# Performance work log

Measured on AMD Instinct MI355X. Metric: run time of the kernel, lower is better.

The kernel has to match this reference:

```python
import jax, jax.numpy as jnp
from jax import lax
import numpy as np

B = 16
H0 = 56
W0 = 56
C = 768
HEADS = 12
SCALES = 3
WS = 7
LC = C // SCALES          # 256 local channels per scale group
HD = C // HEADS           # 64 head dim (= conv groups)
LH = HEADS // SCALES      # 4 local heads per group


def setup_inputs() -> dict:
    key = jax.random.key(0)
    ks = jax.random.split(key, 6)
    x = jax.random.normal(ks[0], (B, H0 * W0, C), jnp.float32)
    w_qkv = jax.random.normal(ks[1], (3 * C, C), jnp.float32) * 0.02
    w_proj = jax.random.normal(ks[2], (C, C), jnp.float32) * 0.02
    b_proj = jnp.zeros((C,), jnp.float32)
    # grouped conv (groups = head_dim = 64): weight (out=LC, in_per_group=LC//HD, 3, 3)
    conv1_w = jax.random.normal(ks[3], (LC, LC // HD, 3, 3), jnp.float32) * 0.05
    conv1_b = jnp.zeros((LC,), jnp.float32)
    conv2_w = jax.random.normal(ks[4], (LC, LC // HD, 3, 3), jnp.float32) * 0.05
    conv2_b = jnp.zeros((LC,), jnp.float32)
    return {"x": x, "w_qkv": w_qkv, "w_proj": w_proj, "b_proj": b_proj,
            "conv1_w": conv1_w, "conv1_b": conv1_b,
            "conv2_w": conv2_w, "conv2_b": conv2_b,
            "H": H0, "W": W0}


def _grouped_conv(xc, w, b, stride, pad, dil):
    y = lax.conv_general_dilated(
        xc, w, window_strides=(stride, stride),
        padding=((pad, pad), (pad, pad)), rhs_dilation=(dil, dil),
        feature_group_count=HD,
        dimension_numbers=("NCHW", "OIHW", "NCHW"))
    return y + b[None, :, None, None]


def _maxpool2(xc):
    return lax.reduce_window(xc, -jnp.inf, lax.max,
                             (1, 1, 2, 2), (1, 1, 2, 2), "VALID")


def _patchify(arr):
    # arr: (B, LC, Hs, Ws) -> (B*n_region, LH, WS*WS, HD)
    b, lc, hs, ws = arr.shape
    a = arr.reshape(b, lc, hs // WS, WS, ws // WS, WS)
    a = a.transpose(0, 2, 4, 3, 5, 1).reshape(-1, WS * WS, lc)
    a = a.reshape(-1, WS * WS, LH, lc // LH).transpose(0, 2, 1, 3)
    return a


def reference(x, w_qkv, w_proj, b_proj, conv1_w, conv1_b, conv2_w, conv2_b, H, W):
    scale = HD ** -0.5
    Bx, N, Cx = x.shape
    # (B, N, 3C) -> (B, H, W, 3, C) -> (B, 3, C, H, W)
    qkv = (x @ w_qkv.T).reshape(Bx, H, W, 3, Cx).transpose(0, 3, 4, 1, 2)
    N_g = (H // WS) * (W // WS)
    conv_params = [(conv1_w, conv1_b, 1, 1, 1), (conv2_w, conv2_b, 2, 2, 2)]
    outs = []
    for i in range(SCALES):
        g = qkv[:, :, i * LC:(i + 1) * LC]  # (B, 3, LC, H, W)
        Hs, Ws = H >> i, W >> i
        if i > 0:
            w, b, st, pd, dl = conv_params[i - 1]
            g = g.reshape(Bx * 3, LC, H, W)
            g = _maxpool2(_grouped_conv(g, w, b, st, pd, dl))
            g = g.reshape(Bx, 3, LC, Hs, Ws)
        q = _patchify(g[:, 0])
        k = _patchify(g[:, 1])
        v = _patchify(g[:, 2])
        attn = jax.nn.softmax(jnp.einsum("whpd,whqd->whpq", q, k) * scale, axis=-1)
        y = jnp.einsum("whpq,whqd->whpd", attn, v)  # (B*nreg, LH, 49, HD)
        nreg = (Hs // WS) * (Ws // WS)
        y = y.reshape(Bx, nreg, LH, WS * WS, HD).transpose(0, 2, 1, 3, 4)
        if i > 0:
            y = jnp.tile(y, (1, 1, N_g // nreg, 1, 1))
        outs.append(y)
    fused = jnp.concatenate(outs, axis=1)  # (B, HEADS, N_g, 49, HD)
    fused = fused.reshape(Bx, HEADS, -1, HD).transpose(0, 2, 1, 3).reshape(Bx, N, Cx)
    return fused @ w_proj.T + b_proj
```

## Files before the change

### kernel.cpp

```cpp
#include <hip/hip_runtime.h>

typedef __attribute__((ext_vector_type(4))) float f32x4;
typedef __attribute__((ext_vector_type(8))) short bf16x8;
typedef __attribute__((ext_vector_type(4))) unsigned short u16x4;
typedef unsigned short u16;

__device__ static u16   g_xh[(size_t)50176 * 768];
__device__ static u16   g_wqkvh[(size_t)2304 * 768];
__device__ static u16   g_wprojh[(size_t)768 * 768];
__device__ static u16   g_qkv[(size_t)50176 * 2304];
__device__ static u16   g_g1[(size_t)48 * 784 * 256];
__device__ static u16   g_g2[(size_t)48 * 196 * 256];
__device__ static u16   g_fh[(size_t)50176 * 768];

static __device__ __forceinline__ u16 f2bf(float x){
  unsigned u = __float_as_uint(x);
  u += 0x7fffu + ((u >> 16) & 1u);
  return (u16)(u >> 16);
}
static __device__ __forceinline__ float bf2f(u16 h){
  return __uint_as_float(((unsigned)h) << 16);
}

__global__ __launch_bounds__(256)
void cvt_bf16(const float* __restrict__ in, u16* __restrict__ out, int n4)
{
  int i = blockIdx.x * blockDim.x + threadIdx.x;
  const int stride = gridDim.x * blockDim.x;
  for (; i < n4; i += stride) {
    const f32x4 v = ((const f32x4*)in)[i];
    u16x4 o;
    #pragma unroll
    for (int j = 0; j < 4; j++) o[j] = f2bf(v[j]);
    ((u16x4*)out)[i] = o;
  }
}

template<bool BIAS, typename OUT_T>
__global__ __launch_bounds__(512, 2)
void gemm256(const u16* __restrict__ A0, const u16* __restrict__ Bw,
             const float* __restrict__ bias, OUT_T* __restrict__ C,
             int N, int K, int GX)
{
  __shared__ __align__(16) char ldsb[4 * 32768];
  const int tid = threadIdx.x;
  const int lane = tid & 63;
  const int w = tid >> 6;
  const int wm = w >> 2;
  const int wn = w & 3;
  const int l15 = lane & 15, l4 = lane >> 4;

  const int nwg = gridDim.x;
  const int bid = blockIdx.x;
  const int q8 = nwg >> 3, r8 = nwg & 7;
  const int xcd = bid & 7, lid = bid >> 3;
  const int swz = (xcd < r8 ? xcd * (q8 + 1) : r8 * (q8 + 1) + (xcd - r8) * q8) + lid;
  const int bn = swz % GX;
  const int bm = swz / GX;

  const int sq = tid >> 3;
  const int sp = tid & 7;
  const int tt = sp ^ (sq & 7);
  const int sa = tt >> 2, scc = tt & 3;
  const int srow0 = sq * 2 + sa;
  const u16* a0 = A0 + (size_t)(bm * 256 + srow0) * K + scc * 8;
  const u16* a1 = A0 + (size_t)(bm * 256 + 128 + srow0) * K + scc * 8;
  const u16* b0 = Bw + (size_t)(bn * 256 + srow0) * K + scc * 8;
  const u16* b1 = Bw + (size_t)(bn * 256 + 128 + srow0) * K + scc * 8;
  const int wofs = w << 10;

  #define GLDS(srcp, ldsoff) __builtin_amdgcn_global_load_lds( \
      (__attribute__((address_space(1))) const void*)(srcp),   \
      (__attribute__((address_space(3))) void*)(ldsb + (ldsoff)), 16, 0, 0)

  auto STAGE = [&](int s) {
    const int bb = (s & 3) << 15;
    const int ko = s * 32;
    GLDS(a0 + ko, bb + wofs);
    GLDS(a1 + ko, bb + 8192 + wofs);
    GLDS(b0 + ko, bb + 16384 + wofs);
    GLDS(b1 + ko, bb + 24576 + wofs);
  };

  f32x4 acc[8][4];
  #pragma unroll
  for (int i = 0; i < 8; i++)
    #pragma unroll
    for (int j = 0; j < 4; j++) acc[i][j] = (f32x4)0.f;

  auto COMPUTE = [&](int t) {
    const char* base = ldsb + ((t & 3) << 15);
    bf16x8 bfr[4], afr[8];
    #pragma unroll
    for (int ni = 0; ni < 4; ni++) {
      const int r = wn * 64 + ni * 16 + l15;
      const int pr = r >> 1;
      const int p = (((r & 1) << 2) + l4) ^ (pr & 7);
      bfr[ni] = *(const bf16x8*)(base + 16384 + pr * 128 + p * 16);
    }
    #pragma unroll
    for (int mi = 0; mi < 8; mi++) {
      const int r = wm * 128 + mi * 16 + l15;
      const int pr = r >> 1;
      const int p = (((r & 1) << 2) + l4) ^ (pr & 7);
      afr[mi] = *(const bf16x8*)(base + pr * 128 + p * 16);
    }
    __builtin_amdgcn_s_setprio(1);
    #pragma unroll
    for (int mi = 0; mi < 8; mi++)
      #pragma unroll
      for (int ni = 0; ni < 4; ni++)
        acc[mi][ni] = __builtin_amdgcn_mfma_f32_16x16x32_bf16(afr[mi], bfr[ni], acc[mi][ni], 0, 0, 0);
    __builtin_amdgcn_s_setprio(0);
  };

  const int T = K >> 5;
  STAGE(0);
  STAGE(1);
  for (int t = 0; t < T - 2; ++t) {
    STAGE(t + 2);
    asm volatile("s_waitcnt vmcnt(8)" ::: "memory");
    __builtin_amdgcn_sched_barrier(0);
    __builtin_amdgcn_s_barrier();
    __builtin_amdgcn_sched_barrier(0);
    COMPUTE(t);
  }
  asm volatile("s_waitcnt vmcnt(4)" ::: "memory");
  __builtin_amdgcn_sched_barrier(0);
  __builtin_amdgcn_s_barrier();
  __builtin_amdgcn_sched_barrier(0);
  COMPUTE(T - 2);
  asm volatile("s_waitcnt vmcnt(0)" ::: "memory");
  __builtin_amdgcn_sched_barrier(0);
  __builtin_amdgcn_s_barrier();
  __builtin_amdgcn_sched_barrier(0);
  COMPUTE(T - 1);
  #undef GLDS

  #pragma unroll
  for (int mi = 0; mi < 8; mi++)
    #pragma unroll
    for (int ni = 0; ni < 4; ni++) {
      const int col = bn * 256 + wn * 64 + ni * 16 + l15;
      const float bv = BIAS ? bias[col] : 0.f;
      #pragma unroll
      for (int reg = 0; reg < 4; reg++) {
        const int row = bm * 256 + wm * 128 + mi * 16 + (l4 << 2) + reg;
        const float val = acc[mi][ni][reg] + bv;
        if constexpr (sizeof(OUT_T) == 2) C[(size_t)row * N + col] = (OUT_T)f2bf(val);
        else                              C[(size_t)row * N + col] = val;
      }
    }
}

__global__ __launch_bounds__(256)
void conv_pool(const u16* __restrict__ qkv, const float* __restrict__ wsrc,
               const float* __restrict__ bias, u16* __restrict__ gout,
               int chan0, int Pout, int st, int pd, int dl)
{
  __shared__ float wl[64 * 145];
  const int g = threadIdx.x;
  const int ty = threadIdx.y;
  const int tid = ty * 64 + g;
  for (int i = tid; i < 9216; i += 256) {
    const int oc = i / 36, rem = i - oc * 36;
    wl[(oc >> 2) * 145 + (oc & 3) * 36 + rem] = wsrc[i];
  }
  __syncthreads();

  const int bt = blockIdx.x;
  const int b = bt / 3, t = bt - b * 3;
  const int total = Pout * Pout;
  const int p = blockIdx.y * 4 + ty;
  if (p >= total) return;
  const int y = p / Pout, x = p - y * Pout;

  const f32x4 bias4 = *(const f32x4*)&bias[g * 4];
  f32x4 best;
  #pragma unroll
  for (int j = 0; j < 4; j++) best[j] = -3.4e38f;
  const float* wg = &wl[g * 145];

  #pragma unroll
  for (int dy = 0; dy < 2; dy++)
    #pragma unroll
    for (int dx = 0; dx < 2; dx++) {
      const int py = 2 * y + dy, px = 2 * x + dx;
      f32x4 c4 = bias4;
      #pragma unroll
      for (int ky = 0; ky < 3; ky++) {
        const int iy = py * st - pd + ky * dl;
        if (iy < 0 || iy >= 56) continue;
        #pragma unroll
        for (int kx = 0; kx < 3; kx++) {
          const int ix = px * st - pd + kx * dl;
          if (ix < 0 || ix >= 56) continue;
          const u16x4 in4 = *(const u16x4*)&qkv[(size_t)(b * 3136 + iy * 56 + ix) * 2304 + t * 768 + chan0 + g * 4];
          const float f0 = bf2f(in4[0]), f1 = bf2f(in4[1]), f2 = bf2f(in4[2]), f3 = bf2f(in4[3]);
          #pragma unroll
          for (int oc = 0; oc < 4; oc++) {
            const float* wp = &wg[oc * 36 + ky * 3 + kx];
            c4[oc] += f0 * wp[0] + f1 * wp[9] + f2 * wp[18] + f3 * wp[27];
          }
        }
      }
      #pragma unroll
      for (int j = 0; j < 4; j++) best[j] = fmaxf(best[j], c4[j]);
    }
  u16x4 o4;
  #pragma unroll
  for (int j = 0; j < 4; j++) o4[j] = f2bf(best[j]);
  *(u16x4*)&gout[((size_t)bt * total + p) * 256 + g * 4] = o4;
}

template<int SRC>
__global__ __launch_bounds__(256)
void attn_mfma(const u16* __restrict__ src, u16* __restrict__ fh,
               int side, int Hs, int head_base, int rep)
{
  __shared__ __align__(16) u16 sV[4][64 * 64];
  __shared__ __align__(16) u16 sP[4][64 * 64];
  const int tid = threadIdx.x;
  const int lane = tid & 63;
  const int w = tid >> 6;
  const int nreg = side * side;
  int unit = blockIdx.x * 4 + w;
  const int h = unit & 3; unit >>= 2;
  const int r = unit % nreg;
  const int b = unit / nreg;
  const int hr = r / side, wr = r - hr * side;
  const int l15 = lane & 15, l4 = lane >> 4;

  char* vb = (char*)sV[w];
  char* pb = (char*)sP[w];

  auto gidx = [&](int t, int pp, int c) -> size_t {
    const int py = pp / 7, px = pp - py * 7;
    const int yy = hr * 7 + py, xx = wr * 7 + px;
    if (SRC == 0) return ((size_t)(b * 3136 + yy * 56 + xx)) * 2304 + (size_t)(t * 768 + h * 64 + c);
    else          return ((size_t)(b * 3 + t)) * ((size_t)Hs * Hs * 256) + (size_t)(yy * Hs + xx) * 256 + h * 64 + c;
  };

  for (int i = lane; i < 1024; i += 64) {
    const int q = i >> 4, dc = i & 15;
    const int qs = q > 48 ? 48 : q;
    const u16x4 v4 = *(const u16x4*)&src[gidx(2, qs, dc * 4)];
    *(u16x4*)(vb + ((q * 128 + dc * 8) ^ (((q >> 3) & 3) << 5))) = v4;
  }

  f32x4 s[4][4];
  #pragma unroll
  for (int i = 0; i < 4; i++)
    #pragma unroll
    for (int j = 0; j < 4; j++) s[i][j] = (f32x4)0.f;

  bf16x8 bk[4][2];
  #pragma unroll
  for (int ni = 0; ni < 4; ni++) {
    const int q = ni * 16 + l15;
    const int qs = q > 48 ? 48 : q;
    #pragma unroll
    for (int ks = 0; ks < 2; ks++)
      bk[ni][ks] = *(const bf16x8*)&src[gidx(1, qs, ks * 32 + l4 * 8)];
  }
  #pragma unroll
  for (int mi = 0; mi < 4; mi++) {
    const int p = mi * 16 + l15;
    const int ps = p > 48 ? 48 : p;
    const bf16x8 a0 = *(const bf16x8*)&src[gidx(0, ps, l4 * 8)];
    const bf16x8 a1 = *(const bf16x8*)&src[gidx(0, ps, 32 + l4 * 8)];
    #pragma unroll
    for (int ni = 0; ni < 4; ni++) {
      s[mi][ni] = __builtin_amdgcn_mfma_f32_16x16x32_bf16(a0, bk[ni][0], s[mi][ni], 0, 0, 0);
      s[mi][ni] = __builtin_amdgcn_mfma_f32_16x16x32_bf16(a1, bk[ni][1], s[mi][ni], 0, 0, 0);
    }
  }

  #pragma unroll
  for (int ni = 0; ni < 4; ni++) {
    const bool bad = (ni * 16 + l15) > 48;
    #pragma unroll
    for (int mi = 0; mi < 4; mi++)
      #pragma unroll
      for (int reg = 0; reg < 4; reg++)
        s[mi][ni][reg] = bad ? -1e30f : s[mi][ni][reg];
  }

  float inv[4][4];
  #pragma unroll
  for (int mi = 0; mi < 4; mi++)
    #pragma unroll
    for (int reg = 0; reg < 4; reg++) {
      float m = fmaxf(fmaxf(s[mi][0][reg], s[mi][1][reg]), fmaxf(s[mi][2][reg], s[mi][3][reg]));
      m = fmaxf(m, __shfl_xor(m, 1));
      m = fmaxf(m, __shfl_xor(m, 2));
      m = fmaxf(m, __shfl_xor(m, 4));
      m = fmaxf(m, __shfl_xor(m, 8));
      float partial = 0.f;
      #pragma unroll
      for (int ni = 0; ni < 4; ni++) {
        const float e = __expf((s[mi][ni][reg] - m) * 0.125f);
        s[mi][ni][reg] = e;
        partial += e;
      }
      partial += __shfl_xor(partial, 1);
      partial += __shfl_xor(partial, 2);
      partial += __shfl_xor(partial, 4);
      partial += __shfl_xor(partial, 8);
      inv[mi][reg] = 1.f / partial;
    }

  #pragma unroll
  for (int mi = 0; mi < 4; mi++)
    #pragma unroll
    for (int ni = 0; ni < 4; ni++)
      #pragma unroll
      for (int reg = 0; reg < 4; reg++) {
        const int row = mi * 16 + l4 * 4 + reg;
        const int col = ni * 16 + l15;
        *(u16*)(pb + ((row * 128 + col * 2) ^ ((row & 7) << 4))) = f2bf(s[mi][ni][reg]);
      }
  __syncthreads();

  f32x4 o[4][4];
  #pragma unroll
  for (int i = 0; i < 4; i++)
    #pragma unroll
    for (int j = 0; j < 4; j++) o[i][j] = (f32x4)0.f;

  #pragma unroll
  for (int ks = 0; ks < 2; ks++) {
    bf16x8 bv[4];
    #pragma unroll
    for (int ni = 0; ni < 4; ni++)
      #pragma unroll
      for (int j = 0; j < 8; j++) {
        const int q = ks * 32 + l4 * 8 + j;
        bv[ni][j] = *(const short*)(vb + ((q * 128 + (ni * 16 + l15) * 2) ^ (((q >> 3) & 3) << 5)));
      }
    #pragma unroll
    for (int mi = 0; mi < 4; mi++) {
      const int row = mi * 16 + l15;
      const bf16x8 pa = *(const bf16x8*)(pb + ((row * 128 + (ks * 4 + l4) * 16) ^ ((row & 7) << 4)));
      #pragma unroll
      for (int ni = 0; ni < 4; ni++)
        o[mi][ni] = __builtin_amdgcn_mfma_f32_16x16x32_bf16(pa, bv[ni], o[mi][ni], 0, 0, 0);
    }
  }

  const int head = head_base + h;
  #pragma unroll
  for (int mi = 0; mi < 4; mi++)
    #pragma unroll
    for (int reg = 0; reg < 4; reg++) {
      const int p = mi * 16 + l4 * 4 + reg;
      if (p >= 49) continue;
      const float iv = inv[mi][reg];
      u16 hv[4];
      #pragma unroll
      for (int ni = 0; ni < 4; ni++) hv[ni] = f2bf(o[mi][ni][reg] * iv);
      for (int m = 0; m < rep; m++) {
        const size_t ob = ((size_t)b * 3136 + (size_t)(m * nreg + r) * 49 + p) * 768 + head * 64 + l15;
        #pragma unroll
        for (int ni = 0; ni < 4; ni++) fh[ob + ni * 16] = hv[ni];
      }
    }
}

extern "C" void kernel_launch(void* const* d_in, const int* in_sizes, int n_in,
                              void* d_out, int out_size, void* d_ws, size_t ws_size,
                              hipStream_t stream)
{
  const float* x      = (const float*)d_in[0];
  const float* w_qkv  = (const float*)d_in[1];
  const float* w_proj = (const float*)d_in[2];
  const float* b_proj = (const float*)d_in[3];
  const float* c1w    = (const float*)d_in[4];
  const float* c1b    = (const float*)d_in[5];
  const float* c2w    = (const float*)d_in[6];
  const float* c2b    = (const float*)d_in[7];
  float* out = (float*)d_out;

  u16 *xh, *wqkvh, *wprojh, *qkvb, *g1, *g2, *fh;
  hipGetSymbolAddress((void**)&xh,     HIP_SYMBOL(g_xh));
  hipGetSymbolAddress((void**)&wqkvh,  HIP_SYMBOL(g_wqkvh));
  hipGetSymbolAddress((void**)&wprojh, HIP_SYMBOL(g_wprojh));
  hipGetSymbolAddress((void**)&qkvb,   HIP_SYMBOL(g_qkv));
  hipGetSymbolAddress((void**)&g1,     HIP_SYMBOL(g_g1));
  hipGetSymbolAddress((void**)&g2,     HIP_SYMBOL(g_g2));
  hipGetSymbolAddress((void**)&fh,     HIP_SYMBOL(g_fh));

  cvt_bf16<<<2048, 256, 0, stream>>>(x,      xh,     50176 * 768 / 4);
  cvt_bf16<<<512,  256, 0, stream>>>(w_qkv,  wqkvh,  2304 * 768 / 4);
  cvt_bf16<<<512,  256, 0, stream>>>(w_proj, wprojh, 768 * 768 / 4);

  gemm256<false, u16><<<(50176 / 256) * (2304 / 256), 512, 0, stream>>>(
      xh, wqkvh, nullptr, qkvb, 2304, 768, 2304 / 256);

  conv_pool<<<dim3(48, 196), dim3(64, 4), 0, stream>>>(qkvb, c1w, c1b, g1, 256, 28, 1, 1, 1);
  conv_pool<<<dim3(48, 49),  dim3(64, 4), 0, stream>>>(qkvb, c2w, c2b, g2, 512, 14, 2, 2, 2);

  attn_mfma<0><<<16 * 64 * 4 / 4, 256, 0, stream>>>(qkvb, fh, 8, 56, 0, 1);
  attn_mfma<1><<<16 * 16 * 4 / 4, 256, 0, stream>>>(g1,   fh, 4, 28, 4, 4);
  attn_mfma<1><<<16 * 4 * 4 / 4,  256, 0, stream>>>(g2,   fh, 2, 14, 8, 16);

  gemm256<true, float><<<(50176 / 256) * (768 / 256), 512, 0, stream>>>(
      fh, wprojh, b_proj, out, 768, 768, 768 / 256);
}
```

Before: 628.1 us.

## Restructure GEMM into 8-slot half-tile pipeline and specialize stride-1 conv-pool

Replaces the 4-stage K=32 GEMM pipeline with an 8-slot ring of half-tiles at K=64. Loads are issued one quarter-step at a time, interleaved with MFMA phases, and the M/N warp mapping is interleaved. The aim is finer-grained overlap of global-to-LDS traffic with matrix math. It also adds a specialized stride-1 conv+maxpool kernel that loads a 4x4 input patch once into registers, so the four pooled positions reuse shared inputs instead of reloading them. The cost is more barriers per K step and extra register pressure.

```diff
diff --git a/kernel.cpp b/kernel.cpp
--- a/kernel.cpp
+++ b/kernel.cpp
@@ -38,11 +38,11 @@
 
 template<bool BIAS, typename OUT_T>
 __global__ __launch_bounds__(512, 2)
-void gemm256(const u16* __restrict__ A0, const u16* __restrict__ Bw,
-             const float* __restrict__ bias, OUT_T* __restrict__ C,
-             int N, int K, int GX)
-{
-  __shared__ __align__(16) char ldsb[4 * 32768];
+void gemm8p(const u16* __restrict__ A0, const u16* __restrict__ Bw,
+            const float* __restrict__ bias, OUT_T* __restrict__ C,
+            int N, int K, int GX)
+{
+  __shared__ __align__(16) char ldsb[8 * 16384];
   const int tid = threadIdx.x;
   const int lane = tid & 63;
   const int w = tid >> 6;
@@ -58,99 +58,181 @@
   const int bn = swz % GX;
   const int bm = swz / GX;
 
-  const int sq = tid >> 3;
-  const int sp = tid & 7;
-  const int tt = sp ^ (sq & 7);
-  const int sa = tt >> 2, scc = tt & 3;
-  const int srow0 = sq * 2 + sa;
-  const u16* a0 = A0 + (size_t)(bm * 256 + srow0) * K + scc * 8;
-  const u16* a1 = A0 + (size_t)(bm * 256 + 128 + srow0) * K + scc * 8;
-  const u16* b0 = Bw + (size_t)(bn * 256 + srow0) * K + scc * 8;
-  const u16* b1 = Bw + (size_t)(bn * 256 + 128 + srow0) * K + scc * 8;
-  const int wofs = w << 10;
+  const int T = K >> 6;
 
   #define GLDS(srcp, ldsoff) __builtin_amdgcn_global_load_lds( \
       (__attribute__((address_space(1))) const void*)(srcp),   \
       (__attribute__((address_space(3))) void*)(ldsb + (ldsoff)), 16, 0, 0)
 
-  auto STAGE = [&](int s) {
-    const int bb = (s & 3) << 15;
-    const int ko = s * 32;
-    GLDS(a0 + ko, bb + wofs);
-    GLDS(a1 + ko, bb + 8192 + wofs);
-    GLDS(b0 + ko, bb + 16384 + wofs);
-    GLDS(b1 + ko, bb + 24576 + wofs);
+  auto stage_half = [&](int h) {
+    if (h >= 4 * T) return;
+    const int t = h >> 2, kind = h & 3;
+    const int slot = (h & 7) << 14;
+    #pragma unroll
+    for (int j = 0; j < 2; j++) {
+      const int prow = (tid >> 3) + (j << 6);
+      const int c8 = (tid & 7) ^ (prow & 7);
+      const int col = (t << 6) + (c8 << 3);
+      const u16* src;
+      if (kind < 2) src = Bw + (size_t)(bn * 256 + (kind << 7) + prow) * K + col;
+      else          src = A0 + (size_t)(bm * 256 + ((kind - 2) << 7) + prow) * K + col;
+      GLDS(src, slot + (j << 13) + tid * 16);
+    }
   };
 
+  auto frag = [&](int base, int rbase, int ks) -> bf16x8 {
+    const int row = rbase + l15;
+    return *(const bf16x8*)(ldsb + base + row * 128 + ((((ks << 2) + l4) ^ (row & 7)) << 4));
+  };
+
   f32x4 acc[8][4];
   #pragma unroll
   for (int i = 0; i < 8; i++)
     #pragma unroll
     for (int j = 0; j < 4; j++) acc[i][j] = (f32x4)0.f;
 
-  auto COMPUTE = [&](int t) {
-    const char* base = ldsb + ((t & 3) << 15);
-    bf16x8 bfr[4], afr[8];
-    #pragma unroll
-    for (int ni = 0; ni < 4; ni++) {
-      const int r = wn * 64 + ni * 16 + l15;
-      const int pr = r >> 1;
-      const int p = (((r & 1) << 2) + l4) ^ (pr & 7);
-      bfr[ni] = *(const bf16x8*)(base + 16384 + pr * 128 + p * 16);
-    }
-    #pragma unroll
-    for (int mi = 0; mi < 8; mi++) {
-      const int r = wm * 128 + mi * 16 + l15;
-      const int pr = r >> 1;
-      const int p = (((r & 1) << 2) + l4) ^ (pr & 7);
-      afr[mi] = *(const bf16x8*)(base + pr * 128 + p * 16);
-    }
-    __builtin_amdgcn_s_setprio(1);
-    #pragma unroll
-    for (int mi = 0; mi < 8; mi++)
-      #pragma unroll
-      for (int ni = 0; ni < 4; ni++)
-        acc[mi][ni] = __builtin_amdgcn_mfma_f32_16x16x32_bf16(afr[mi], bfr[ni], acc[mi][ni], 0, 0, 0);
-    __builtin_amdgcn_s_setprio(0);
-  };
-
-  const int T = K >> 5;
-  STAGE(0);
-  STAGE(1);
-  for (int t = 0; t < T - 2; ++t) {
-    STAGE(t + 2);
-    asm volatile("s_waitcnt vmcnt(8)" ::: "memory");
-    __builtin_amdgcn_sched_barrier(0);
-    __builtin_amdgcn_s_barrier();
-    __builtin_amdgcn_sched_barrier(0);
-    COMPUTE(t);
-  }
-  asm volatile("s_waitcnt vmcnt(4)" ::: "memory");
+  #pragma unroll
+  for (int h = 0; h < 7; h++) stage_half(h);
+  asm volatile("s_waitcnt vmcnt(6)" ::: "memory");
   __builtin_amdgcn_sched_barrier(0);
   __builtin_amdgcn_s_barrier();
   __builtin_amdgcn_sched_barrier(0);
-  COMPUTE(T - 2);
-  asm volatile("s_waitcnt vmcnt(0)" ::: "memory");
-  __builtin_amdgcn_sched_barrier(0);
-  __builtin_amdgcn_s_barrier();
-  __builtin_amdgcn_sched_barrier(0);
-  COMPUTE(T - 1);
+
+  bf16x8 bfr[4][2];
+
+  for (int t = 0; t < T; ++t) {
+    const int pb = (t & 1) << 16;
+    #pragma unroll
+    for (int p = 0; p < 4; p++) {
+      bf16x8 afr[2][2];
+      #pragma unroll
+      for (int j = 0; j < 2; j++) {
+        const int r = wm * 16 + (2 * p + j) * 32;
+        const int abase = pb + ((r >> 7) ? 49152 : 32768);
+        const int pr = r & 127;
+        #pragma unroll
+        for (int ks = 0; ks < 2; ks++) afr[j][ks] = frag(abase, pr, ks);
+      }
+      if (p == 0) {
+        #pragma unroll
+        for (int ni = 0; ni < 4; ni++) {
+          const int r = wn * 16 + ni * 64;
+          const int bbase = pb + ((r >> 7) ? 16384 : 0);
+          const int pr = r & 127;
+          #pragma unroll
+          for (int ks = 0; ks < 2; ks++) bfr[ni][ks] = frag(bbase, pr, ks);
+        }
+      }
+      stage_half(4 * t + p + 7);
+      if (p == 3) {
+        if (t == T - 2) {
+          asm volatile("s_waitcnt vmcnt(0)" ::: "memory");
+        } else if (t < T - 2) {
+          asm volatile("s_waitcnt vmcnt(6)" ::: "memory");
+        }
+      }
+      __builtin_amdgcn_sched_barrier(0);
+      __builtin_amdgcn_s_barrier();
+      __builtin_amdgcn_sched_barrier(0);
+      asm volatile("s_waitcnt lgkmcnt(0)" ::: "memory");
+      __builtin_amdgcn_sched_barrier(0);
+      __builtin_amdgcn_s_setprio(1);
+      #pragma unroll
+      for (int j = 0; j < 2; j++)
+        #pragma unroll
+        for (int ks = 0; ks < 2; ks++)
+          #pragma unroll
+          for (int ni = 0; ni < 4; ni++)
+            acc[2 * p + j][ni] = __builtin_amdgcn_mfma_f32_16x16x32_bf16(
+                afr[j][ks], bfr[ni][ks], acc[2 * p + j][ni], 0, 0, 0);
+      __builtin_amdgcn_s_setprio(0);
+      __builtin_amdgcn_sched_barrier(0);
+      __builtin_amdgcn_s_barrier();
+      __builtin_amdgcn_sched_barrier(0);
+    }
+  }
   #undef GLDS
 
   #pragma unroll
   for (int mi = 0; mi < 8; mi++)
     #pragma unroll
     for (int ni = 0; ni < 4; ni++) {
-      const int col = bn * 256 + wn * 64 + ni * 16 + l15;
+      const int col = bn * 256 + wn * 16 + ni * 64 + l15;
       const float bv = BIAS ? bias[col] : 0.f;
       #pragma unroll
       for (int reg = 0; reg < 4; reg++) {
-        const int row = bm * 256 + wm * 128 + mi * 16 + (l4 << 2) + reg;
+        const int row = bm * 256 + wm * 16 + mi * 32 + (l4 << 2) + reg;
         const float val = acc[mi][ni][reg] + bv;
         if constexpr (sizeof(OUT_T) == 2) C[(size_t)row * N + col] = (OUT_T)f2bf(val);
         else                              C[(size_t)row * N + col] = val;
       }
     }
+}
+
+__global__ __launch_bounds__(256)
+void conv_pool1(const u16* __restrict__ qkv, const float* __restrict__ wsrc,
+                const float* __restrict__ bias, u16* __restrict__ gout)
+{
+  __shared__ float wl[64 * 145];
+  const int g = threadIdx.x;
+  const int ty = threadIdx.y;
+  const int tid = ty * 64 + g;
+  for (int i = tid; i < 9216; i += 256) {
+    const int oc = i / 36, rem = i - oc * 36;
+    wl[(oc >> 2) * 145 + (oc & 3) * 36 + rem] = wsrc[i];
+  }
+  __syncthreads();
+
+  const int bt = blockIdx.x;
+  const int b = bt / 3, t = bt - b * 3;
+  const int p = blockIdx.y * 4 + ty;
+  const int y = p / 28, x = p - y * 28;
+  const float* wg = &wl[g * 145];
+
+  f32x4 f[4][4];
+  #pragma unroll
+  for (int i = 0; i < 4; i++) {
+    const int iy = 2 * y - 1 + i;
+    #pragma unroll
+    for (int k = 0; k < 4; k++) {
+      const int ix = 2 * x - 1 + k;
+      f32x4 v = (f32x4)0.f;
+      if (iy >= 0 && iy < 56 && ix >= 0 && ix < 56) {
+        const u16x4 in4 = *(const u16x4*)&qkv[(size_t)(b * 3136 + iy * 56 + ix) * 2304 + t * 768 + 256 + g * 4];
+        v[0] = bf2f(in4[0]); v[1] = bf2f(in4[1]); v[2] = bf2f(in4[2]); v[3] = bf2f(in4[3]);
+      }
+      f[i][k] = v;
+    }
+  }
+
+  const f32x4 bias4 = *(const f32x4*)&bias[g * 4];
+  f32x4 best;
+  #pragma unroll
+  for (int j = 0; j < 4; j++) best[j] = -3.4e38f;
+
+  #pragma unroll
+  for (int dy = 0; dy < 2; dy++)
+    #pragma unroll
+    for (int dx = 0; dx < 2; dx++) {
+      f32x4 c4 = bias4;
+      #pragma unroll
+      for (int ky = 0; ky < 3; ky++)
+        #pragma unroll
+        for (int kx = 0; kx < 3; kx++) {
+          const f32x4 in4 = f[dy + ky][dx + kx];
+          #pragma unroll
+          for (int oc = 0; oc < 4; oc++) {
+            const float* wp = &wg[oc * 36 + ky * 3 + kx];
+            c4[oc] += in4[0] * wp[0] + in4[1] * wp[9] + in4[2] * wp[18] + in4[3] * wp[27];
+          }
+        }
+      #pragma unroll
+      for (int j = 0; j < 4; j++) best[j] = fmaxf(best[j], c4[j]);
+    }
+  u16x4 o4;
+  #pragma unroll
+  for (int j = 0; j < 4; j++) o4[j] = f2bf(best[j]);
+  *(u16x4*)&gout[((size_t)bt * 784 + p) * 256 + g * 4] = o4;
 }
 
 __global__ __launch_bounds__(256)
@@ -394,16 +476,16 @@
   cvt_bf16<<<512,  256, 0, stream>>>(w_qkv,  wqkvh,  2304 * 768 / 4);
   cvt_bf16<<<512,  256, 0, stream>>>(w_proj, wprojh, 768 * 768 / 4);
 
-  gemm256<false, u16><<<(50176 / 256) * (2304 / 256), 512, 0, stream>>>(
+  gemm8p<false, u16><<<(50176 / 256) * (2304 / 256), 512, 0, stream>>>(
       xh, wqkvh, nullptr, qkvb, 2304, 768, 2304 / 256);
 
-  conv_pool<<<dim3(48, 196), dim3(64, 4), 0, stream>>>(qkvb, c1w, c1b, g1, 256, 28, 1, 1, 1);
+  conv_pool1<<<dim3(48, 196), dim3(64, 4), 0, stream>>>(qkvb, c1w, c1b, g1);
   conv_pool<<<dim3(48, 49),  dim3(64, 4), 0, stream>>>(qkvb, c2w, c2b, g2, 512, 14, 2, 2, 2);
 
   attn_mfma<0><<<16 * 64 * 4 / 4, 256, 0, stream>>>(qkvb, fh, 8, 56, 0, 1);
   attn_mfma<1><<<16 * 16 * 4 / 4, 256, 0, stream>>>(g1,   fh, 4, 28, 4, 4);
   attn_mfma<1><<<16 * 4 * 4 / 4,  256, 0, stream>>>(g2,   fh, 2, 14, 8, 16);
 
-  gemm256<true, float><<<(50176 / 256) * (768 / 256), 512, 0, stream>>>(
+  gemm8p<true, float><<<(50176 / 256) * (768 / 256), 512, 0, stream>>>(
       fh, wprojh, b_proj, out, 768, 768, 768 / 256);
 }
```

New measurement: 653.7 us. 1.04x slower.

## Merge conversion, conv and attention launches into single grid kernels

Applied to the files above, without the earlier changes.

Combines the three bf16 conversion launches into one kernel, the two conv+maxpool launches into one grid split by blockIdx.y, and the three attention launches into one grid split by block index. This removes launch gaps and tail underutilization between the small kernels. For the stride-1 conv branch it also preloads a 4x4 input patch into registers and reuses it across the four pooled positions instead of reloading overlapping inputs. The cost is added register pressure and branch divergence inside the merged kernels.

```diff
diff --git a/kernel.cpp b/kernel.cpp
--- a/kernel.cpp
+++ b/kernel.cpp
@@ -23,16 +23,23 @@
 }
 
 __global__ __launch_bounds__(256)
-void cvt_bf16(const float* __restrict__ in, u16* __restrict__ out, int n4)
-{
+void cvt_bf16_3(const float* __restrict__ i0, u16* __restrict__ o0, int n0,
+                const float* __restrict__ i1, u16* __restrict__ o1, int n1,
+                const float* __restrict__ i2, u16* __restrict__ o2, int n2)
+{
+  const int total = n0 + n1 + n2;
   int i = blockIdx.x * blockDim.x + threadIdx.x;
   const int stride = gridDim.x * blockDim.x;
-  for (; i < n4; i += stride) {
-    const f32x4 v = ((const f32x4*)in)[i];
+  for (; i < total; i += stride) {
+    const float* in; u16* out; int j = i;
+    if (j < n0)           { in = i0; out = o0; }
+    else if (j < n0 + n1) { in = i1; out = o1; j -= n0; }
+    else                  { in = i2; out = o2; j -= n0 + n1; }
+    const f32x4 v = ((const f32x4*)in)[j];
     u16x4 o;
     #pragma unroll
-    for (int j = 0; j < 4; j++) o[j] = f2bf(v[j]);
-    ((u16x4*)out)[i] = o;
+    for (int k = 0; k < 4; k++) o[k] = f2bf(v[k]);
+    ((u16x4*)out)[j] = o;
   }
 }
 
@@ -154,85 +161,130 @@
 }
 
 __global__ __launch_bounds__(256)
-void conv_pool(const u16* __restrict__ qkv, const float* __restrict__ wsrc,
-               const float* __restrict__ bias, u16* __restrict__ gout,
-               int chan0, int Pout, int st, int pd, int dl)
+void conv_all(const u16* __restrict__ qkv,
+              const float* __restrict__ c1w, const float* __restrict__ c1b,
+              u16* __restrict__ g1,
+              const float* __restrict__ c2w, const float* __restrict__ c2b,
+              u16* __restrict__ g2)
 {
   __shared__ float wl[64 * 145];
   const int g = threadIdx.x;
   const int ty = threadIdx.y;
   const int tid = ty * 64 + g;
+  const int bt = blockIdx.x;
+  const int b = bt / 3, t = bt - b * 3;
+  const bool is1 = blockIdx.y < 196;
+
+  const float* wsrc = is1 ? c1w : c2w;
   for (int i = tid; i < 9216; i += 256) {
     const int oc = i / 36, rem = i - oc * 36;
     wl[(oc >> 2) * 145 + (oc & 3) * 36 + rem] = wsrc[i];
   }
   __syncthreads();
-
-  const int bt = blockIdx.x;
-  const int b = bt / 3, t = bt - b * 3;
-  const int total = Pout * Pout;
-  const int p = blockIdx.y * 4 + ty;
-  if (p >= total) return;
-  const int y = p / Pout, x = p - y * Pout;
-
-  const f32x4 bias4 = *(const f32x4*)&bias[g * 4];
-  f32x4 best;
-  #pragma unroll
-  for (int j = 0; j < 4; j++) best[j] = -3.4e38f;
   const float* wg = &wl[g * 145];
 
-  #pragma unroll
-  for (int dy = 0; dy < 2; dy++)
-    #pragma unroll
-    for (int dx = 0; dx < 2; dx++) {
-      const int py = 2 * y + dy, px = 2 * x + dx;
-      f32x4 c4 = bias4;
-      #pragma unroll
-      for (int ky = 0; ky < 3; ky++) {
-        const int iy = py * st - pd + ky * dl;
-        if (iy < 0 || iy >= 56) continue;
+  if (is1) {
+    const int p = blockIdx.y * 4 + ty;
+    const int y = p / 28, x = p - y * 28;
+
+    f32x4 f[4][4];
+    #pragma unroll
+    for (int i = 0; i < 4; i++) {
+      const int iy = 2 * y - 1 + i;
+      #pragma unroll
+      for (int k = 0; k < 4; k++) {
+        const int ix = 2 * x - 1 + k;
+        f32x4 v = (f32x4)0.f;
+        if (iy >= 0 && iy < 56 && ix >= 0 && ix < 56) {
+          const u16x4 in4 = *(const u16x4*)&qkv[(size_t)(b * 3136 + iy * 56 + ix) * 2304 + t * 768 + 256 + g * 4];
+          v[0] = bf2f(in4[0]); v[1] = bf2f(in4[1]); v[2] = bf2f(in4[2]); v[3] = bf2f(in4[3]);
+        }
+        f[i][k] = v;
+      }
+    }
+
+    const f32x4 bias4 = *(const f32x4*)&c1b[g * 4];
+    f32x4 best;
+    #pragma unroll
+    for (int j = 0; j < 4; j++) best[j] = -3.4e38f;
+
+    #pragma unroll
+    for (int dy = 0; dy < 2; dy++)
+      #pragma unroll
+      for (int dx = 0; dx < 2; dx++) {
+        f32x4 c4 = bias4;
         #pragma unroll
-        for (int kx = 0; kx < 3; kx++) {
-          const int ix = px * st - pd + kx * dl;
-          if (ix < 0 || ix >= 56) continue;
-          const u16x4 in4 = *(const u16x4*)&qkv[(size_t)(b * 3136 + iy * 56 + ix) * 2304 + t * 768 + chan0 + g * 4];
-          const float f0 = bf2f(in4[0]), f1 = bf2f(in4[1]), f2 = bf2f(in4[2]), f3 = bf2f(in4[3]);
+        for (int ky = 0; ky < 3; ky++)
           #pragma unroll
-          for (int oc = 0; oc < 4; oc++) {
-            const float* wp = &wg[oc * 36 + ky * 3 + kx];
-            c4[oc] += f0 * wp[0] + f1 * wp[9] + f2 * wp[18] + f3 * wp[27];
+          for (int kx = 0; kx < 3; kx++) {
+            const f32x4 in4 = f[dy + ky][dx + kx];
+            #pragma unroll
+            for (int oc = 0; oc < 4; oc++) {
+              const float* wp = &wg[oc * 36 + ky * 3 + kx];
+              c4[oc] += in4[0] * wp[0] + in4[1] * wp[9] + in4[2] * wp[18] + in4[3] * wp[27];
+            }
+          }
+        #pragma unroll
+        for (int j = 0; j < 4; j++) best[j] = fmaxf(best[j], c4[j]);
+      }
+    u16x4 o4;
+    #pragma unroll
+    for (int j = 0; j < 4; j++) o4[j] = f2bf(best[j]);
+    *(u16x4*)&g1[((size_t)bt * 784 + p) * 256 + g * 4] = o4;
+  } else {
+    const int p = (blockIdx.y - 196) * 4 + ty;
+    const int y = p / 14, x = p - y * 14;
+
+    const f32x4 bias4 = *(const f32x4*)&c2b[g * 4];
+    f32x4 best;
+    #pragma unroll
+    for (int j = 0; j < 4; j++) best[j] = -3.4e38f;
+
+    #pragma unroll
+    for (int dy = 0; dy < 2; dy++)
+      #pragma unroll
+      for (int dx = 0; dx < 2; dx++) {
+        const int py = 2 * y + dy, px = 2 * x + dx;
+        f32x4 c4 = bias4;
+        #pragma unroll
+        for (int ky = 0; ky < 3; ky++) {
+          const int iy = py * 2 - 2 + ky * 2;
+          if (iy < 0 || iy >= 56) continue;
+          #pragma unroll
+          for (int kx = 0; kx < 3; kx++) {
+            const int ix = px * 2 - 2 + kx * 2;
+            if (ix < 0 || ix >= 56) continue;
+            const u16x4 in4 = *(const u16x4*)&qkv[(size_t)(b * 3136 + iy * 56 + ix) * 2304 + t * 768 + 512 + g * 4];
+            const float f0 = bf2f(in4[0]), f1 = bf2f(in4[1]), f2 = bf2f(in4[2]), f3 = bf2f(in4[3]);
+            #pragma unroll
+            for (int oc = 0; oc < 4; oc++) {
+              const float* wp = &wg[oc * 36 + ky * 3 + kx];
+              c4[oc] += f0 * wp[0] + f1 * wp[9] + f2 * wp[18] + f3 * wp[27];
+            }
           }
         }
-      }
-      #pragma unroll
-      for (int j = 0; j < 4; j++) best[j] = fmaxf(best[j], c4[j]);
-    }
-  u16x4 o4;
-  #pragma unroll
-  for (int j = 0; j < 4; j++) o4[j] = f2bf(best[j]);
-  *(u16x4*)&gout[((size_t)bt * total + p) * 256 + g * 4] = o4;
+        #pragma unroll
+        for (int j = 0; j < 4; j++) best[j] = fmaxf(best[j], c4[j]);
+      }
+    u16x4 o4;
+    #pragma unroll
+    for (int j = 0; j < 4; j++) o4[j] = f2bf(best[j]);
+    *(u16x4*)&g2[((size_t)bt * 196 + p) * 256 + g * 4] = o4;
+  }
 }
 
 template<int SRC>
-__global__ __launch_bounds__(256)
-void attn_mfma(const u16* __restrict__ src, u16* __restrict__ fh,
-               int side, int Hs, int head_base, int rep)
-{
-  __shared__ __align__(16) u16 sV[4][64 * 64];
-  __shared__ __align__(16) u16 sP[4][64 * 64];
-  const int tid = threadIdx.x;
-  const int lane = tid & 63;
-  const int w = tid >> 6;
+static __device__ __forceinline__
+void attn_body(const u16* __restrict__ src, u16* __restrict__ fh,
+               int side, int Hs, int head_base, int rep,
+               int unit, int lane, char* vb, char* pb)
+{
   const int nreg = side * side;
-  int unit = blockIdx.x * 4 + w;
   const int h = unit & 3; unit >>= 2;
   const int r = unit % nreg;
   const int b = unit / nreg;
   const int hr = r / side, wr = r - hr * side;
   const int l15 = lane & 15, l4 = lane >> 4;
-
-  char* vb = (char*)sV[w];
-  char* pb = (char*)sP[w];
 
   auto gidx = [&](int t, int pp, int c) -> size_t {
     const int py = pp / 7, px = pp - py * 7;
@@ -365,6 +417,28 @@
         for (int ni = 0; ni < 4; ni++) fh[ob + ni * 16] = hv[ni];
       }
     }
+}
+
+__global__ __launch_bounds__(256)
+void attn_all(const u16* __restrict__ qkv, const u16* __restrict__ g1,
+              const u16* __restrict__ g2, u16* __restrict__ fh)
+{
+  __shared__ __align__(16) u16 sV[4][64 * 64];
+  __shared__ __align__(16) u16 sP[4][64 * 64];
+  const int tid = threadIdx.x;
+  const int lane = tid & 63;
+  const int w = tid >> 6;
+  char* vb = (char*)sV[w];
+  char* pb = (char*)sP[w];
+  const int bid = blockIdx.x;
+
+  if (bid < 1024) {
+    attn_body<0>(qkv, fh, 8, 56, 0, 1,  bid * 4 + w,          lane, vb, pb);
+  } else if (bid < 1280) {
+    attn_body<1>(g1,  fh, 4, 28, 4, 4,  (bid - 1024) * 4 + w, lane, vb, pb);
+  } else {
+    attn_body<1>(g2,  fh, 2, 14, 8, 16, (bid - 1280) * 4 + w, lane, vb, pb);
+  }
 }
 
 extern "C" void kernel_launch(void* const* d_in, const int* in_sizes, int n_in,
@@ -390,19 +464,16 @@
   hipGetSymbolAddress((void**)&g2,     HIP_SYMBOL(g_g2));
   hipGetSymbolAddress((void**)&fh,     HIP_SYMBOL(g_fh));
 
-  cvt_bf16<<<2048, 256, 0, stream>>>(x,      xh,     50176 * 768 / 4);
-  cvt_bf16<<<512,  256, 0, stream>>>(w_qkv,  wqkvh,  2304 * 768 / 4);
-  cvt_bf16<<<512,  256, 0, stream>>>(w_proj, wprojh, 768 * 768 / 4);
+  cvt_bf16_3<<<2048, 256, 0, stream>>>(x, xh, 50176 * 768 / 4,
+                                       w_qkv, wqkvh, 2304 * 768 / 4,
+                                       w_proj, wprojh, 768 * 768 / 4);
 
   gemm256<false, u16><<<(50176 / 256) * (2304 / 256), 512, 0, stream>>>(
       xh, wqkvh, nullptr, qkvb, 2304, 768, 2304 / 256);
 
-  conv_pool<<<dim3(48, 196), dim3(64, 4), 0, stream>>>(qkvb, c1w, c1b, g1, 256, 28, 1, 1, 1);
-  conv_pool<<<dim3(48, 49),  dim3(64, 4), 0, stream>>>(qkvb, c2w, c2b, g2, 512, 14, 2, 2, 2);
-
-  attn_mfma<0><<<16 * 64 * 4 / 4, 256, 0, stream>>>(qkvb, fh, 8, 56, 0, 1);
-  attn_mfma<1><<<16 * 16 * 4 / 4, 256, 0, stream>>>(g1,   fh, 4, 28, 4, 4);
-  attn_mfma<1><<<16 * 4 * 4 / 4,  256, 0, stream>>>(g2,   fh, 2, 14, 8, 16);
+  conv_all<<<dim3(48, 245), dim3(64, 4), 0, stream>>>(qkvb, c1w, c1b, g1, c2w, c2b, g2);
+
+  attn_all<<<1024 + 256 + 64, 256, 0, stream>>>(qkvb, g1, g2, fh);
 
   gemm256<true, float><<<(50176 / 256) * (768 / 256), 512, 0, stream>>>(
       fh, wprojh, b_proj, out, 768, 768, 768 / 256);
```

Result: no change. 616.1 us (-1.9%).
